# Kernel optimization log

Hardware: AMD Instinct MI355X
Metric: run time of the kernel (lower is better)

## Reference

```python
import jax, jax.numpy as jnp
import numpy as np

DIM = 1024
HEADS = 16
DIM_HEADS = 64
INNER = HEADS * DIM_HEADS
SCALE = (DIM / HEADS) ** (-0.5)  # == DIM_HEADS**-0.5 here
EPS = 1e-5


def setup_inputs() -> dict:
    key = jax.random.key(0)
    k1, k2, k3, k4 = jax.random.split(key, 4)
    x = jax.random.normal(k1, (2, 2048, DIM), dtype=jnp.float32)
    gamma = jnp.ones((DIM,), dtype=jnp.float32)
    beta = jnp.zeros((DIM,), dtype=jnp.float32)
    w_qkv = jax.random.normal(k2, (DIM, 3 * INNER), dtype=jnp.float32) * (DIM ** -0.5)
    w_out = jax.random.normal(k3, (INNER, DIM), dtype=jnp.float32) * (INNER ** -0.5)
    b_out = jax.random.normal(k4, (DIM,), dtype=jnp.float32) * 0.02
    return {"x": x, "gamma": gamma, "beta": beta, "w_qkv": w_qkv,
            "w_out": w_out, "b_out": b_out}


def reference(x, gamma, beta, w_qkv, w_out, b_out):
    # LayerNorm over last dim
    mu = jnp.mean(x, axis=-1, keepdims=True)
    var = jnp.var(x, axis=-1, keepdims=True)
    xn = (x - mu) * jax.lax.rsqrt(var + EPS) * gamma + beta
    # QKV projection (no bias)
    qkv = xn @ w_qkv                                   # [b, n, 3*inner]
    q, k, v = jnp.split(qkv, 3, axis=-1)
    def split_heads(t):
        b, n, _ = t.shape
        return t.reshape(b, n, HEADS, DIM_HEADS).transpose(0, 2, 1, 3)  # [b,h,n,d]
    q, k, v = map(split_heads, (q, k, v))
    dots = jnp.einsum('bhid,bhjd->bhij', q, k) * SCALE  # [b,h,n,n]
    att = jax.nn.softmax(dots, axis=-1)
    sa = jnp.einsum('bhij,bhjd->bhid', att, v)          # [b,h,n,d]
    b, h, n, d = sa.shape
    out = sa.transpose(0, 2, 1, 3).reshape(b, n, h * d)  # [b,n,inner]
    return out @ w_out + b_out
```

## Files before the change

### kernel.cpp

```cpp
#include <hip/hip_runtime.h>

typedef __attribute__((ext_vector_type(4))) float f32x4;
typedef __attribute__((ext_vector_type(16))) float f32x16;
typedef __attribute__((ext_vector_type(8))) __bf16 bf16x8;
typedef __attribute__((ext_vector_type(4))) unsigned short u16x4;
typedef __attribute__((ext_vector_type(2))) unsigned int u32x2;

#define DEVI static __device__ __forceinline__

DEVI unsigned short bf16_bits(float f) {
  __bf16 h = (__bf16)f;
  return __builtin_bit_cast(unsigned short, h);
}

DEVI void gl_lds16(const void* g, void* l) {
  __builtin_amdgcn_global_load_lds(
      (const __attribute__((address_space(1))) void*)g,
      (__attribute__((address_space(3))) void*)l, 16, 0, 0);
}

DEVI f32x4 mfma16x16(bf16x8 a, bf16x8 b, f32x4 c) {
  return __builtin_amdgcn_mfma_f32_16x16x32_bf16(a, b, c, 0, 0, 0);
}

DEVI f32x16 mfma32(bf16x8 a, bf16x8 b, f32x16 c) {
  return __builtin_amdgcn_mfma_f32_32x32x16_bf16(a, b, c, 0, 0, 0);
}

DEVI unsigned cvtpk_bf16(float lo, float hi2) {
  unsigned r;
  asm("v_cvt_pk_bf16_f32 %0, %1, %2" : "=v"(r) : "v"(lo), "v"(hi2));
  return r;
}

DEVI void pl32swap(unsigned& a, unsigned& b) {
  asm volatile("s_nop 1\nv_permlane32_swap_b32 %0, %1\ns_nop 1"
               : "+v"(a), "+v"(b));
}

__global__ __launch_bounds__(256) void ln_kernel(
    const float* __restrict__ x, const float* __restrict__ gamma,
    const float* __restrict__ beta, __bf16* __restrict__ xn) {
  int row = blockIdx.x;
  int t = threadIdx.x;
  float4 v = ((const float4*)(x + (size_t)row * 1024))[t];
  float s = v.x + v.y + v.z + v.w;
  float sq = v.x * v.x + v.y * v.y + v.z * v.z + v.w * v.w;
#pragma unroll
  for (int off = 32; off > 0; off >>= 1) {
    s += __shfl_down(s, off);
    sq += __shfl_down(sq, off);
  }
  __shared__ float red[8];
  int w = t >> 6, ln = t & 63;
  if (ln == 0) { red[w] = s; red[4 + w] = sq; }
  __syncthreads();
  s = red[0] + red[1] + red[2] + red[3];
  sq = red[4] + red[5] + red[6] + red[7];
  float mu = s * (1.0f / 1024.0f);
  float var = sq * (1.0f / 1024.0f) - mu * mu;
  float rstd = rsqrtf(var + 1e-5f);
  float4 g = ((const float4*)gamma)[t];
  float4 b = ((const float4*)beta)[t];
  u16x4 o;
  o[0] = bf16_bits((v.x - mu) * rstd * g.x + b.x);
  o[1] = bf16_bits((v.y - mu) * rstd * g.y + b.y);
  o[2] = bf16_bits((v.z - mu) * rstd * g.z + b.z);
  o[3] = bf16_bits((v.w - mu) * rstd * g.w + b.w);
  *(u16x4*)(xn + (size_t)row * 1024 + t * 4) = o;
}

__global__ __launch_bounds__(256) void transpose_bf16_kernel(
    const float* __restrict__ in, __bf16* __restrict__ out, int R, int C) {
  __shared__ float tile[64][65];
  int tx = threadIdx.x & 15, ty = threadIdx.x >> 4;
  int c0 = blockIdx.x * 64, r0 = blockIdx.y * 64;
#pragma unroll
  for (int p = 0; p < 4; ++p) {
    int r = ty + p * 16;
    float4 v = *(const float4*)(in + (size_t)(r0 + r) * C + c0 + tx * 4);
    tile[r][tx * 4 + 0] = v.x;
    tile[r][tx * 4 + 1] = v.y;
    tile[r][tx * 4 + 2] = v.z;
    tile[r][tx * 4 + 3] = v.w;
  }
  __syncthreads();
#pragma unroll
  for (int p = 0; p < 4; ++p) {
    int cc = ty + p * 16;
    u16x4 o;
    o[0] = bf16_bits(tile[tx * 4 + 0][cc]);
    o[1] = bf16_bits(tile[tx * 4 + 1][cc]);
    o[2] = bf16_bits(tile[tx * 4 + 2][cc]);
    o[3] = bf16_bits(tile[tx * 4 + 3][cc]);
    *(u16x4*)(out + (size_t)(c0 + cc) * R + r0 + tx * 4) = o;
  }
}

template <int EPI>
__global__ __launch_bounds__(256) void gemm_kernel(
    const __bf16* __restrict__ A, const __bf16* __restrict__ BT,
    float* __restrict__ Cout, const float* __restrict__ bias,
    __bf16* __restrict__ Qb, __bf16* __restrict__ Kb, __bf16* __restrict__ VTb) {
  __shared__ __align__(16) __bf16 Asm[128 * 32];
  __shared__ __align__(16) __bf16 Bsm[128 * 32];
  const int KD = 1024;
  int t = threadIdx.x;
  int w = t >> 6, ln = t & 63;
  int wr = w >> 1, wc = w & 1;
  int m0 = blockIdx.y * 128, n0 = blockIdx.x * 128;
  f32x4 acc[4][4] = {};

  int srow = w * 16 + (ln >> 2);
  int scol = (ln & 3) * 8;
  int lrow = ln & 15;
  int lkb = (ln >> 4) * 16;

  for (int kk = 0; kk < KD; kk += 32) {
    __syncthreads();
#pragma unroll
    for (int i = 0; i < 2; ++i) {
      int row = i * 64 + srow;
      gl_lds16(A + (size_t)(m0 + row) * KD + kk + scol,
               (char*)Asm + i * 4096 + w * 1024);
      gl_lds16(BT + (size_t)(n0 + row) * KD + kk + scol,
               (char*)Bsm + i * 4096 + w * 1024);
    }
    __syncthreads();
    bf16x8 af[4], bfr[4];
#pragma unroll
    for (int mi = 0; mi < 4; ++mi)
      af[mi] = *(const bf16x8*)((char*)Asm + (wr * 64 + mi * 16 + lrow) * 64 + lkb);
#pragma unroll
    for (int ni = 0; ni < 4; ++ni)
      bfr[ni] = *(const bf16x8*)((char*)Bsm + (wc * 64 + ni * 16 + lrow) * 64 + lkb);
#pragma unroll
    for (int mi = 0; mi < 4; ++mi)
#pragma unroll
      for (int ni = 0; ni < 4; ++ni)
        acc[mi][ni] = mfma16x16(af[mi], bfr[ni], acc[mi][ni]);
  }

  int r4 = (ln >> 4) * 4;
#pragma unroll
  for (int mi = 0; mi < 4; ++mi) {
#pragma unroll
    for (int ni = 0; ni < 4; ++ni) {
      int grow = m0 + wr * 64 + mi * 16 + r4;
      int gcol = n0 + wc * 64 + ni * 16 + lrow;
      if (EPI == 0) {
        int sel = gcol >> 10;
        int nl = gcol & 1023;
        int h = nl >> 6, d = nl & 63;
        int b = grow >> 11, seq = grow & 2047;
        int bh = b * 16 + h;
        if (sel < 2) {
          __bf16* dst = (sel == 0 ? Qb : Kb) + ((size_t)bh * 2048 + seq) * 64 + d;
#pragma unroll
          for (int r = 0; r < 4; ++r) dst[(size_t)r * 64] = (__bf16)acc[mi][ni][r];
        } else {
          u16x4 o;
          o[0] = bf16_bits(acc[mi][ni][0]);
          o[1] = bf16_bits(acc[mi][ni][1]);
          o[2] = bf16_bits(acc[mi][ni][2]);
          o[3] = bf16_bits(acc[mi][ni][3]);
          *(u16x4*)(VTb + ((size_t)bh * 64 + d) * 2048 + seq) = o;
        }
      } else {
        float bv = bias[gcol];
#pragma unroll
        for (int r = 0; r < 4; ++r)
          Cout[(size_t)(grow + r) * 1024 + gcol] = acc[mi][ni][r] + bv;
      }
    }
  }
}

__global__ __launch_bounds__(256, 2) void attn_kernel(
    const __bf16* __restrict__ Qb, const __bf16* __restrict__ Kb,
    const __bf16* __restrict__ VTb, __bf16* __restrict__ sa) {
  __shared__ __align__(16) char Klds[24576];
  __shared__ __align__(16) char Vlds[24576];
  const float SCALE = 0.125f;
  const float LOG2E = 1.44269504f;
  const float K1 = SCALE * LOG2E;
  int t = threadIdx.x, w = t >> 6, ln = t & 63;
  int hi = ln >> 5, col = ln & 31;
  int bh = blockIdx.y, bq = bh >> 4, h = bh & 15;
  int q0 = blockIdx.x * 128;
  const __bf16* Qh = Qb + (size_t)bh * 2048 * 64;
  const __bf16* Kh = Kb + (size_t)bh * 2048 * 64;
  const __bf16* Vh = VTb + (size_t)bh * 64 * 2048;

  bf16x8 qf[4];
  int qrow = q0 + w * 32 + col;
#pragma unroll
  for (int dk = 0; dk < 4; ++dk)
    qf[dk] = *(const bf16x8*)(Qh + (size_t)qrow * 64 + dk * 16 + hi * 8);

  f32x16 oacc0 = {}, oacc1 = {};
  float m_run = -1e30f, l_run = 0.f;

  int sj0 = t >> 3, sc0 = (t & 7) ^ (sj0 & 7);
  int sj1 = 32 + (t >> 3), sc1 = (t & 7) ^ (sj1 & 7);

#define STAGE(off, j0_)                                                        \
  do {                                                                         \
    gl_lds16(Kh + (size_t)((j0_) + sj0) * 64 + sc0 * 8, Klds + (off) + w * 1024); \
    gl_lds16(Kh + (size_t)((j0_) + sj1) * 64 + sc1 * 8,                        \
             Klds + (off) + 4096 + w * 1024);                                  \
    gl_lds16(Vh + (size_t)sj0 * 2048 + (j0_) + sc0 * 8, Vlds + (off) + w * 1024); \
    gl_lds16(Vh + (size_t)sj1 * 2048 + (j0_) + sc1 * 8,                        \
             Vlds + (off) + 4096 + w * 1024);                                  \
  } while (0)

  STAGE(0, 0);
  STAGE(8192, 64);

  int cb = 0;
  int sb = 2;

  for (int jt = 0; jt < 32; ++jt) {
    if (jt < 31) {
      asm volatile("s_waitcnt vmcnt(4)" ::: "memory");
    } else {
      asm volatile("s_waitcnt vmcnt(0)" ::: "memory");
    }
    __builtin_amdgcn_s_barrier();
    __builtin_amdgcn_sched_barrier(0);

    const char* Kc = Klds + cb * 8192;
    const char* Vc = Vlds + cb * 8192;

    f32x16 sfr0 = {}, sfr1 = {};
#pragma unroll
    for (int dk = 0; dk < 4; ++dk) {
      int sw = ((dk * 32 + hi * 16) ^ ((col & 7) << 4));
      bf16x8 kf0 = *(const bf16x8*)(Kc + col * 128 + sw);
      bf16x8 kf1 = *(const bf16x8*)(Kc + (32 + col) * 128 + sw);
      sfr0 = mfma32(kf0, qf[dk], sfr0);
      sfr1 = mfma32(kf1, qf[dk], sfr1);
    }

    float t8[8];
#pragma unroll
    for (int r = 0; r < 8; ++r)
      t8[r] = fmaxf(fmaxf(sfr0[r], sfr0[r + 8]), fmaxf(sfr1[r], sfr1[r + 8]));
    float mx = fmaxf(fmaxf(fmaxf(t8[0], t8[1]), fmaxf(t8[2], t8[3])),
                     fmaxf(fmaxf(t8[4], t8[5]), fmaxf(t8[6], t8[7])));
    mx = fmaxf(mx, __shfl_xor(mx, 32));
    float pmax = mx * SCALE;

    if (__any(pmax > m_run + 8.0f)) {
      float mnew = fmaxf(m_run, pmax);
      float corr = __builtin_amdgcn_exp2f((m_run - mnew) * LOG2E);
      l_run *= corr;
#pragma unroll
      for (int r = 0; r < 16; ++r) { oacc0[r] *= corr; oacc1[r] *= corr; }
      m_run = mnew;
    }
    float mb = -m_run * LOG2E;

    float psum = 0.f;
    bf16x8 pfr[4];
#pragma unroll
    for (int jk = 0; jk < 4; ++jk) {
      float p[8];
#pragma unroll
      for (int c = 0; c < 8; ++c) {
        float sv = (jk < 2) ? sfr0[(jk & 1) * 8 + c] : sfr1[(jk & 1) * 8 + c];
        p[c] = __builtin_amdgcn_exp2f(fmaf(sv, K1, mb));
      }
      psum += ((p[0] + p[1]) + (p[2] + p[3])) + ((p[4] + p[5]) + (p[6] + p[7]));
      unsigned X0 = cvtpk_bf16(p[0], p[1]);
      unsigned X1 = cvtpk_bf16(p[2], p[3]);
      unsigned Y0 = cvtpk_bf16(p[4], p[5]);
      unsigned Y1 = cvtpk_bf16(p[6], p[7]);
      pl32swap(X0, Y0);
      pl32swap(X1, Y1);
      union { unsigned u[4]; bf16x8 v; } pu;
      pu.u[0] = X0; pu.u[1] = X1; pu.u[2] = Y0; pu.u[3] = Y1;
      pfr[jk] = pu.v;
    }
    psum += __shfl_xor(psum, 32);
    l_run += psum;

#pragma unroll
    for (int jk = 0; jk < 4; ++jk) {
      int sw = ((jk * 32 + hi * 16) ^ ((col & 7) << 4));
      bf16x8 vf0 = *(const bf16x8*)(Vc + col * 128 + sw);
      bf16x8 vf1 = *(const bf16x8*)(Vc + (32 + col) * 128 + sw);
      oacc0 = mfma32(vf0, pfr[jk], oacc0);
      oacc1 = mfma32(vf1, pfr[jk], oacc1);
    }

    if (jt < 30) STAGE(sb * 8192, (jt + 2) * 64);
    cb = (cb == 2) ? 0 : cb + 1;
    sb = (sb == 2) ? 0 : sb + 1;
  }
#undef STAGE

  __syncthreads();
  float linv = 1.0f / l_run;
  char* Ow = Klds + w * 4096;
#pragma unroll
  for (int da = 0; da < 2; ++da) {
    const f32x16& oa = da ? oacc1 : oacc0;
#pragma unroll
    for (int g = 0; g < 4; ++g) {
      unsigned w0 = cvtpk_bf16(oa[g * 4 + 0] * linv, oa[g * 4 + 1] * linv);
      unsigned w1 = cvtpk_bf16(oa[g * 4 + 2] * linv, oa[g * 4 + 3] * linv);
      int dby = da * 64 + g * 16 + hi * 8;
      char* dst = Ow + col * 128 + ((dby & ~15) ^ ((col & 7) << 4)) + (dby & 8);
      u32x2 pr = {w0, w1};
      *(u32x2*)dst = pr;
    }
  }
  int rr0 = ln >> 3, c16o = ln & 7;
#pragma unroll
  for (int pp = 0; pp < 4; ++pp) {
    int rr = rr0 + pp * 8;
    bf16x8 ov = *(const bf16x8*)(Ow + rr * 128 + ((c16o * 16) ^ ((rr & 7) << 4)));
    int grow = bq * 2048 + q0 + w * 32 + rr;
    *(bf16x8*)(sa + (size_t)grow * 1024 + h * 64 + c16o * 8) = ov;
  }
}

extern "C" void kernel_launch(void* const* d_in, const int* in_sizes, int n_in,
                              void* d_out, int out_size, void* d_ws, size_t ws_size,
                              hipStream_t stream) {
  const float* x = (const float*)d_in[0];
  const float* gamma = (const float*)d_in[1];
  const float* beta = (const float*)d_in[2];
  const float* w_qkv = (const float*)d_in[3];
  const float* w_out = (const float*)d_in[4];
  const float* b_out = (const float*)d_in[5];

  char* ws = (char*)d_ws;
  __bf16* xn = (__bf16*)(ws);
  __bf16* wqkvT = (__bf16*)(ws + (8l << 20));
  __bf16* woutT = (__bf16*)(ws + (14l << 20));
  __bf16* Qb = (__bf16*)(ws + (16l << 20));
  __bf16* Kb = (__bf16*)(ws + (24l << 20));
  __bf16* VTb = (__bf16*)(ws + (32l << 20));
  __bf16* sa = xn;

  ln_kernel<<<4096, 256, 0, stream>>>(x, gamma, beta, xn);
  transpose_bf16_kernel<<<dim3(48, 16), 256, 0, stream>>>(w_qkv, wqkvT, 1024, 3072);
  transpose_bf16_kernel<<<dim3(16, 16), 256, 0, stream>>>(w_out, woutT, 1024, 1024);
  gemm_kernel<0><<<dim3(24, 32), 256, 0, stream>>>(xn, wqkvT, nullptr, nullptr,
                                                   Qb, Kb, VTb);
  attn_kernel<<<dim3(16, 32), 256, 0, stream>>>(Qb, Kb, VTb, sa);
  gemm_kernel<1><<<dim3(8, 32), 256, 0, stream>>>(sa, woutT, (float*)d_out, b_out,
                                                  nullptr, nullptr, nullptr);
}
```

Baseline: 127.1 us.

## Software-pipeline QK^T of next tile with softmax and PV of current tile

Restructures the flash-attention inner loop so the QK^T MFMAs for tile j+1 are issued before the softmax and PV work of tile j, using ping-pong score registers and a loop unrolled by two. The aim is to overlap matrix-core work with the exp/max VALU work and hide LDS latency. The prefetch STAGE is moved to the start of each iteration, with a full vmcnt(0) wait before each barrier. This raises register pressure and the stricter wait may expose more global-load latency.

```diff
diff --git a/kernel.cpp b/kernel.cpp
--- a/kernel.cpp
+++ b/kernel.cpp
@@ -214,90 +214,97 @@
              Vlds + (off) + 4096 + w * 1024);                                  \
   } while (0)
 
+#define QK_TILE(SB0, SB1, KBASE)                                               \
+  do {                                                                         \
+    const char* Kc_ = (KBASE);                                                 \
+    SB0 = (f32x16){};                                                          \
+    SB1 = (f32x16){};                                                          \
+    _Pragma("unroll") for (int dk = 0; dk < 4; ++dk) {                         \
+      int sw = ((dk * 32 + hi * 16) ^ ((col & 7) << 4));                       \
+      bf16x8 kf0 = *(const bf16x8*)(Kc_ + col * 128 + sw);                     \
+      bf16x8 kf1 = *(const bf16x8*)(Kc_ + (32 + col) * 128 + sw);              \
+      SB0 = mfma32(kf0, qf[dk], SB0);                                          \
+      SB1 = mfma32(kf1, qf[dk], SB1);                                          \
+    }                                                                          \
+  } while (0)
+
+#define ATTN_ITER(SA0, SA1, SB0, SB1, JT)                                      \
+  do {                                                                         \
+    asm volatile("s_waitcnt vmcnt(0)" ::: "memory");                           \
+    __builtin_amdgcn_s_barrier();                                              \
+    __builtin_amdgcn_sched_barrier(0);                                         \
+    if ((JT) < 30) STAGE(sb * 8192, ((JT) + 2) * 64);                          \
+    if ((JT) < 31) QK_TILE(SB0, SB1, Klds + kb * 8192);                        \
+    float t8[8];                                                               \
+    _Pragma("unroll") for (int r = 0; r < 8; ++r)                              \
+        t8[r] = fmaxf(fmaxf(SA0[r], SA0[r + 8]), fmaxf(SA1[r], SA1[r + 8]));   \
+    float mx = fmaxf(fmaxf(fmaxf(t8[0], t8[1]), fmaxf(t8[2], t8[3])),          \
+                     fmaxf(fmaxf(t8[4], t8[5]), fmaxf(t8[6], t8[7])));         \
+    mx = fmaxf(mx, __shfl_xor(mx, 32));                                        \
+    float pmax = mx * SCALE;                                                   \
+    if (__any(pmax > m_run + 8.0f)) {                                          \
+      float mnew = fmaxf(m_run, pmax);                                         \
+      float corr = __builtin_amdgcn_exp2f((m_run - mnew) * LOG2E);             \
+      l_run *= corr;                                                           \
+      _Pragma("unroll") for (int r = 0; r < 16; ++r) {                         \
+        oacc0[r] *= corr;                                                      \
+        oacc1[r] *= corr;                                                      \
+      }                                                                        \
+      m_run = mnew;                                                            \
+    }                                                                          \
+    float mb = -m_run * LOG2E;                                                 \
+    float psum = 0.f;                                                          \
+    bf16x8 pfr[4];                                                             \
+    _Pragma("unroll") for (int jk = 0; jk < 4; ++jk) {                         \
+      float p[8];                                                              \
+      _Pragma("unroll") for (int c = 0; c < 8; ++c) {                          \
+        float sv = (jk < 2) ? SA0[(jk & 1) * 8 + c] : SA1[(jk & 1) * 8 + c];   \
+        p[c] = __builtin_amdgcn_exp2f(fmaf(sv, K1, mb));                       \
+      }                                                                        \
+      psum += ((p[0] + p[1]) + (p[2] + p[3])) + ((p[4] + p[5]) + (p[6] + p[7]));\
+      unsigned X0 = cvtpk_bf16(p[0], p[1]);                                    \
+      unsigned X1 = cvtpk_bf16(p[2], p[3]);                                    \
+      unsigned Y0 = cvtpk_bf16(p[4], p[5]);                                    \
+      unsigned Y1 = cvtpk_bf16(p[6], p[7]);                                    \
+      pl32swap(X0, Y0);                                                        \
+      pl32swap(X1, Y1);                                                        \
+      union { unsigned u[4]; bf16x8 v; } pu;                                   \
+      pu.u[0] = X0; pu.u[1] = X1; pu.u[2] = Y0; pu.u[3] = Y1;                  \
+      pfr[jk] = pu.v;                                                          \
+    }                                                                          \
+    {                                                                          \
+      const char* Vc_ = Vlds + vb * 8192;                                      \
+      _Pragma("unroll") for (int jk = 0; jk < 4; ++jk) {                       \
+        int sw = ((jk * 32 + hi * 16) ^ ((col & 7) << 4));                     \
+        bf16x8 vf0 = *(const bf16x8*)(Vc_ + col * 128 + sw);                   \
+        bf16x8 vf1 = *(const bf16x8*)(Vc_ + (32 + col) * 128 + sw);            \
+        oacc0 = mfma32(vf0, pfr[jk], oacc0);                                   \
+        oacc1 = mfma32(vf1, pfr[jk], oacc1);                                   \
+      }                                                                        \
+    }                                                                          \
+    psum += __shfl_xor(psum, 32);                                              \
+    l_run += psum;                                                             \
+    vb = (vb == 2) ? 0 : vb + 1;                                               \
+    kb = (kb == 2) ? 0 : kb + 1;                                               \
+    sb = (sb == 2) ? 0 : sb + 1;                                               \
+  } while (0)
+
   STAGE(0, 0);
   STAGE(8192, 64);
-
-  int cb = 0;
-  int sb = 2;
-
-  for (int jt = 0; jt < 32; ++jt) {
-    if (jt < 31) {
-      asm volatile("s_waitcnt vmcnt(4)" ::: "memory");
-    } else {
-      asm volatile("s_waitcnt vmcnt(0)" ::: "memory");
-    }
-    __builtin_amdgcn_s_barrier();
-    __builtin_amdgcn_sched_barrier(0);
-
-    const char* Kc = Klds + cb * 8192;
-    const char* Vc = Vlds + cb * 8192;
-
-    f32x16 sfr0 = {}, sfr1 = {};
-#pragma unroll
-    for (int dk = 0; dk < 4; ++dk) {
-      int sw = ((dk * 32 + hi * 16) ^ ((col & 7) << 4));
-      bf16x8 kf0 = *(const bf16x8*)(Kc + col * 128 + sw);
-      bf16x8 kf1 = *(const bf16x8*)(Kc + (32 + col) * 128 + sw);
-      sfr0 = mfma32(kf0, qf[dk], sfr0);
-      sfr1 = mfma32(kf1, qf[dk], sfr1);
-    }
-
-    float t8[8];
-#pragma unroll
-    for (int r = 0; r < 8; ++r)
-      t8[r] = fmaxf(fmaxf(sfr0[r], sfr0[r + 8]), fmaxf(sfr1[r], sfr1[r + 8]));
-    float mx = fmaxf(fmaxf(fmaxf(t8[0], t8[1]), fmaxf(t8[2], t8[3])),
-                     fmaxf(fmaxf(t8[4], t8[5]), fmaxf(t8[6], t8[7])));
-    mx = fmaxf(mx, __shfl_xor(mx, 32));
-    float pmax = mx * SCALE;
-
-    if (__any(pmax > m_run + 8.0f)) {
-      float mnew = fmaxf(m_run, pmax);
-      float corr = __builtin_amdgcn_exp2f((m_run - mnew) * LOG2E);
-      l_run *= corr;
-#pragma unroll
-      for (int r = 0; r < 16; ++r) { oacc0[r] *= corr; oacc1[r] *= corr; }
-      m_run = mnew;
-    }
-    float mb = -m_run * LOG2E;
-
-    float psum = 0.f;
-    bf16x8 pfr[4];
-#pragma unroll
-    for (int jk = 0; jk < 4; ++jk) {
-      float p[8];
-#pragma unroll
-      for (int c = 0; c < 8; ++c) {
-        float sv = (jk < 2) ? sfr0[(jk & 1) * 8 + c] : sfr1[(jk & 1) * 8 + c];
-        p[c] = __builtin_amdgcn_exp2f(fmaf(sv, K1, mb));
-      }
-      psum += ((p[0] + p[1]) + (p[2] + p[3])) + ((p[4] + p[5]) + (p[6] + p[7]));
-      unsigned X0 = cvtpk_bf16(p[0], p[1]);
-      unsigned X1 = cvtpk_bf16(p[2], p[3]);
-      unsigned Y0 = cvtpk_bf16(p[4], p[5]);
-      unsigned Y1 = cvtpk_bf16(p[6], p[7]);
-      pl32swap(X0, Y0);
-      pl32swap(X1, Y1);
-      union { unsigned u[4]; bf16x8 v; } pu;
-      pu.u[0] = X0; pu.u[1] = X1; pu.u[2] = Y0; pu.u[3] = Y1;
-      pfr[jk] = pu.v;
-    }
-    psum += __shfl_xor(psum, 32);
-    l_run += psum;
-
-#pragma unroll
-    for (int jk = 0; jk < 4; ++jk) {
-      int sw = ((jk * 32 + hi * 16) ^ ((col & 7) << 4));
-      bf16x8 vf0 = *(const bf16x8*)(Vc + col * 128 + sw);
-      bf16x8 vf1 = *(const bf16x8*)(Vc + (32 + col) * 128 + sw);
-      oacc0 = mfma32(vf0, pfr[jk], oacc0);
-      oacc1 = mfma32(vf1, pfr[jk], oacc1);
-    }
-
-    if (jt < 30) STAGE(sb * 8192, (jt + 2) * 64);
-    cb = (cb == 2) ? 0 : cb + 1;
-    sb = (sb == 2) ? 0 : sb + 1;
-  }
+  asm volatile("s_waitcnt vmcnt(4)" ::: "memory");
+  __builtin_amdgcn_s_barrier();
+  __builtin_amdgcn_sched_barrier(0);
+
+  f32x16 sfrA0, sfrA1, sfrB0, sfrB1;
+  QK_TILE(sfrA0, sfrA1, Klds);
+
+  int vb = 0, kb = 1, sb = 2;
+  for (int jt2 = 0; jt2 < 32; jt2 += 2) {
+    ATTN_ITER(sfrA0, sfrA1, sfrB0, sfrB1, jt2);
+    ATTN_ITER(sfrB0, sfrB1, sfrA0, sfrA1, jt2 + 1);
+  }
+#undef ATTN_ITER
+#undef QK_TILE
 #undef STAGE
 
   __syncthreads();
```

Result: no change. 127.4 us (+0.2%).
